# Kernel tuning notes

Hardware: AMD Instinct MI355X
Metric: run time of the kernel (lower is better)

Reference implementation:

```python
import jax, jax.numpy as jnp
import numpy as np

N, E, IN, H, G = 100000, 1600000, 64, 108, 128
N_LAYERS = 2  # hidden_dims=[108,108] -> 1 layer from hidden_dims[1:] + 1 final layer


def setup_inputs() -> dict:
    key = jax.random.key(0)
    ks = jax.random.split(key, 13)
    s = lambda fan_in: 1.0 / np.sqrt(fan_in)
    inp = {
        "nodes_feat": jax.random.normal(ks[0], (N, IN), jnp.float32),
        "edges_feat": jax.random.normal(ks[1], (E, 1), jnp.float32),
        "nodes_num_norm_sqrt": jax.random.uniform(ks[2], (N,), jnp.float32),
        "edges_num_norm_sqrt": jax.random.uniform(ks[3], (E,), jnp.float32),
        "W_emb": jax.random.uniform(ks[4], (IN, H), jnp.float32, -s(IN), s(IN)),
        "b_emb": jax.random.uniform(ks[5], (H,), jnp.float32, -s(IN), s(IN)),
        "pool_W": jax.random.uniform(ks[6], (N_LAYERS, H, H), jnp.float32, -s(H), s(H)),
        "pool_b": jax.random.uniform(ks[7], (N_LAYERS, H), jnp.float32, -s(H), s(H)),
        "app_W": jax.random.uniform(ks[8], (N_LAYERS, 2 * H, H), jnp.float32, -s(2 * H), s(2 * H)),
        "app_b": jax.random.uniform(ks[9], (N_LAYERS, H), jnp.float32, -s(2 * H), s(2 * H)),
        "src": jax.random.randint(ks[10], (E,), 0, N, jnp.int64 if jax.config.jax_enable_x64 else jnp.int32),
        "dst": jax.random.randint(ks[11], (E,), 0, N, jnp.int64 if jax.config.jax_enable_x64 else jnp.int32),
        "graph_ids": jnp.sort(jax.random.randint(ks[12], (N,), 0, G, jnp.int64 if jax.config.jax_enable_x64 else jnp.int32)),
        "n_graphs": G,
    }
    return inp


def reference(nodes_feat, edges_feat, nodes_num_norm_sqrt, edges_num_norm_sqrt,
              W_emb, b_emb, pool_W, pool_b, app_W, app_b,
              src, dst, graph_ids, n_graphs):
    n = nodes_feat.shape[0]
    # embedding_h
    h = nodes_feat @ W_emb + b_emb  # [N, H]
    # in-degree for mean aggregation (dropout = 0.0 so omitted)
    deg = jax.ops.segment_sum(jnp.ones((src.shape[0],), h.dtype), dst, num_segments=n)
    deg = jnp.maximum(deg, 1.0)[:, None]  # [N, 1]
    for i in range(pool_W.shape[0]):
        h_in = h
        # meanpool aggregator: per-message linear+ReLU == per-node transform then gather
        z = jax.nn.relu(h @ pool_W[i] + pool_b[i])  # [N, H]
        c = jax.ops.segment_sum(z[src], dst, num_segments=n) / deg  # mean over neighbors
        # NodeApply: linear(concat(h, c)) -> L2 normalize -> activation
        b = jnp.concatenate([h, c], axis=1) @ app_W[i] + app_b[i]
        b = b / jnp.maximum(jnp.linalg.norm(b, axis=1, keepdims=True), 1e-12)
        h = h_in + jax.nn.relu(b)  # residual (dims match: 108 == 108)
    # dgl.mean_nodes readout per graph
    cnt = jax.ops.segment_sum(jnp.ones((n,), h.dtype), graph_ids, num_segments=n_graphs)
    hg = jax.ops.segment_sum(h, graph_ids, num_segments=n_graphs) / jnp.maximum(cnt, 1.0)[:, None]
    return hg  # [n_graphs, H]
```

## Files before the change

kernel.cpp:

```cpp
#include <hip/hip_runtime.h>

#define HDIM 108
constexpr int G_GRAPHS = 128;
constexpr int MAXNB = 1024;
constexpr int CAP = 2560;

typedef _Float16 half8 __attribute__((ext_vector_type(8)));
typedef _Float16 half4v __attribute__((ext_vector_type(4)));
typedef float floatx4 __attribute__((ext_vector_type(4)));
typedef float floatx2 __attribute__((ext_vector_type(2)));

__device__ inline unsigned char f32_to_fp8(float t) {
#if __has_builtin(__builtin_amdgcn_cvt_pk_fp8_f32)
  return (unsigned char)(__builtin_amdgcn_cvt_pk_fp8_f32(t, t, 0, false) & 0xFF);
#else
  t = fminf(t, 448.f);
  if (t < 0.015625f) return (unsigned char)__float2int_rn(t * 512.f);
  unsigned u = __float_as_uint(t);
  unsigned lsb = (u >> 20) & 1;
  u += 0x7FFFFu + lsb;
  int e = (int)((u >> 23) & 0xFF) - 127;
  if (e > 8) return 0x7E;
  return (unsigned char)(((e + 7) << 3) | ((u >> 20) & 7));
#endif
}

template <bool HI>
__device__ inline floatx2 fp8x2_to_f32(unsigned v) {
#if __has_builtin(__builtin_amdgcn_cvt_pk_f32_fp8)
  return __builtin_amdgcn_cvt_pk_f32_fp8((int)v, HI);
#else
  unsigned b0 = HI ? ((v >> 16) & 0xFF) : (v & 0xFF);
  unsigned b1 = HI ? ((v >> 24) & 0xFF) : ((v >> 8) & 0xFF);
  floatx2 r;
  {
    unsigned s = b0 >> 7, e = (b0 >> 3) & 0xF, m = b0 & 7;
    float f = (e == 0) ? (float)m * 0.001953125f
                       : __uint_as_float(((e + 120u) << 23) | (m << 20));
    r[0] = s ? -f : f;
  }
  {
    unsigned s = b1 >> 7, e = (b1 >> 3) & 0xF, m = b1 & 7;
    float f = (e == 0) ? (float)m * 0.001953125f
                       : __uint_as_float(((e + 120u) << 23) | (m << 20));
    r[1] = s ? -f : f;
  }
  return r;
#endif
}

__global__ __launch_bounds__(1024) void k_scatter(const int* __restrict__ src, const int* __restrict__ dst,
                                                  int* __restrict__ gcur, int* __restrict__ ebuf,
                                                  const float* __restrict__ W_emb,
                                                  const float* __restrict__ pool_W,
                                                  const float* __restrict__ app_W,
                                                  _Float16* __restrict__ wte,
                                                  _Float16* __restrict__ wtp,
                                                  _Float16* __restrict__ wta,
                                                  int E, int nb) {
  __shared__ int hist[MAXNB];
  const int tid = threadIdx.x;
  const int e0 = blockIdx.x * 16384;

  int gi = blockIdx.x * 1024 + tid;
  if (gi < 86016) {
    const float* srcw;
    _Float16* dstw;
    int Kpad, K, split, rel;
    if (gi < 7168)       { rel = gi;          srcw = W_emb;          dstw = wte;         Kpad = 64;  K = 64;  split = 0; }
    else if (gi < 21504) { rel = gi - 7168;   srcw = pool_W;         dstw = wtp;         Kpad = 128; K = 108; split = 0; }
    else if (gi < 35840) { rel = gi - 21504;  srcw = pool_W + 11664; dstw = wtp + 14336; Kpad = 128; K = 108; split = 0; }
    else if (gi < 60928) { rel = gi - 35840;  srcw = app_W;          dstw = wta;         Kpad = 224; K = 216; split = 1; }
    else                 { rel = gi - 60928;  srcw = app_W + 23328;  dstw = wta + 25088; Kpad = 224; K = 216; split = 1; }
    int n = rel / Kpad, k = rel - n * Kpad;
    int ks;
    if (split) ks = (k < 108) ? k : (k >= 112 && k < 220) ? (k - 4) : -1;
    else       ks = (k < K) ? k : -1;
    float v = (n < 108 && ks >= 0) ? srcw[ks * 108 + n] : 0.f;
    dstw[rel] = (_Float16)v;
  }

  for (int b = tid; b < nb; b += 1024) hist[b] = 0;
  __syncthreads();
#pragma unroll
  for (int it = 0; it < 16; it++) {
    int e = e0 + it * 1024 + tid;
    if (e < E) atomicAdd(&hist[dst[e] >> 7], 1);
  }
  __syncthreads();
  for (int b = tid; b < nb; b += 1024) {
    int h = hist[b];
    hist[b] = h ? atomicAdd(&gcur[b * 16], h) : 0;
  }
  __syncthreads();
#pragma unroll
  for (int it = 0; it < 16; it++) {
    int e = e0 + it * 1024 + tid;
    if (e < E) {
      int d = dst[e];
      int b = d >> 7;
      int rank = atomicAdd(&hist[b], 1);
      if (rank < CAP) ebuf[(size_t)b * CAP + rank] = src[e] | ((d & 127) << 20);
    }
  }
}

__global__ __launch_bounds__(1024) void k_bagg(const unsigned char* __restrict__ z, const int* __restrict__ ebuf,
                                               const int* __restrict__ gcur, _Float16* __restrict__ c16,
                                               int N, int nb) {
  __shared__ int cnts[128];
  __shared__ int scanb[128];
  __shared__ int off[129];
  __shared__ int ecur[128];
  __shared__ int esrc[CAP];
  const int tid = threadIdx.x;
  const int b = blockIdx.x;
  const int v0 = b << 7;
  int cntb = gcur[b * 16];
  if (cntb > CAP) cntb = CAP;
  const int* eb = ebuf + (size_t)b * CAP;

  if (tid < 128) cnts[tid] = 0;
  __syncthreads();
  for (int i = tid; i < cntb; i += 1024) atomicAdd(&cnts[eb[i] >> 20], 1);
  __syncthreads();
  if (tid < 128) scanb[tid] = cnts[tid];
  __syncthreads();
#pragma unroll
  for (int st = 1; st < 128; st <<= 1) {
    int v = 0;
    if (tid < 128 && tid >= st) v = scanb[tid - st];
    __syncthreads();
    if (tid < 128) scanb[tid] += v;
    __syncthreads();
  }
  if (tid == 0) off[0] = 0;
  if (tid < 128) {
    off[tid + 1] = scanb[tid];
    ecur[tid] = scanb[tid] - cnts[tid];
  }
  __syncthreads();
  for (int i = tid; i < cntb; i += 1024) {
    int e = eb[i];
    int p = atomicAdd(&ecur[e >> 20], 1);
    esrc[p] = e & 0xFFFFF;
  }
  __syncthreads();

  const int lane = tid & 31;
  const int grp = tid >> 5;
  if (lane >= 28) return;
  const unsigned char* __restrict__ zl = z + lane * 4;
#pragma unroll 1
  for (int r = grp; r < 128; r += 32) {
    int v = v0 + r;
    if (v >= N) continue;
    int s = off[r], e2 = off[r + 1];
    float a0 = 0.f, a1 = 0.f, a2 = 0.f, a3 = 0.f;
    int j = s;
    for (; j + 4 <= e2; j += 4) {
      unsigned q0 = *(const unsigned*)(zl + (size_t)esrc[j] * 128);
      unsigned q1 = *(const unsigned*)(zl + (size_t)esrc[j + 1] * 128);
      unsigned q2 = *(const unsigned*)(zl + (size_t)esrc[j + 2] * 128);
      unsigned q3 = *(const unsigned*)(zl + (size_t)esrc[j + 3] * 128);
      floatx2 l0 = fp8x2_to_f32<false>(q0), h0 = fp8x2_to_f32<true>(q0);
      floatx2 l1 = fp8x2_to_f32<false>(q1), h1 = fp8x2_to_f32<true>(q1);
      floatx2 l2 = fp8x2_to_f32<false>(q2), h2 = fp8x2_to_f32<true>(q2);
      floatx2 l3 = fp8x2_to_f32<false>(q3), h3 = fp8x2_to_f32<true>(q3);
      a0 += (l0[0] + l1[0]) + (l2[0] + l3[0]);
      a1 += (l0[1] + l1[1]) + (l2[1] + l3[1]);
      a2 += (h0[0] + h1[0]) + (h2[0] + h3[0]);
      a3 += (h0[1] + h1[1]) + (h2[1] + h3[1]);
    }
    for (; j < e2; j++) {
      unsigned q0 = *(const unsigned*)(zl + (size_t)esrc[j] * 128);
      floatx2 l0 = fp8x2_to_f32<false>(q0), h0 = fp8x2_to_f32<true>(q0);
      a0 += l0[0]; a1 += l0[1]; a2 += h0[0]; a3 += h0[1];
    }
    int d = e2 - s;
    float inv = 1.f / (float)(d > 0 ? d : 1);
    half4v r4;
    r4[0] = (_Float16)(a0 * inv); r4[1] = (_Float16)(a1 * inv);
    r4[2] = (_Float16)(a2 * inv); r4[3] = (_Float16)(a3 * inv);
    *(half4v*)(c16 + (size_t)v * 112 + lane * 4) = r4;
  }
}

template <int KCH, int MODE>
__global__ __launch_bounds__(256) void k_mmf(const void* Asrc, const _Float16* __restrict__ c16,
                                             const _Float16* __restrict__ Wt, const float* __restrict__ bias,
                                             void* outp, int N) {
  constexpr int KW = KCH * 32;
  __shared__ _Float16 As[64 * 40];
  __shared__ _Float16 Ws[112 * 40];

  const int tid = threadIdx.x;
  const int wave = tid >> 6;
  const int lane = tid & 63;
  const int lo = lane & 15;
  const int quad = lane >> 4;
  const int n0 = blockIdx.x * 64;
  const _Float16* h16 = (const _Float16*)Asrc;
  const float* feat = (const float*)Asrc;

  floatx4 acc[7];
#pragma unroll
  for (int ct = 0; ct < 7; ct++) {
    floatx4 zz = {0.f, 0.f, 0.f, 0.f};
    acc[ct] = zz;
  }

#pragma unroll 1
  for (int kc = 0; kc < KCH; kc++) {
    {
      int r = tid >> 2, sg = tid & 3;
      int gn = n0 + r;
      int k = kc * 32 + sg * 8;
      half8 v = {0, 0, 0, 0, 0, 0, 0, 0};
      if (gn < N) {
        if (MODE == 0) {
          float4 f0 = *(const float4*)(feat + (size_t)gn * 64 + k);
          float4 f1 = *(const float4*)(feat + (size_t)gn * 64 + k + 4);
          v[0] = (_Float16)f0.x; v[1] = (_Float16)f0.y; v[2] = (_Float16)f0.z; v[3] = (_Float16)f0.w;
          v[4] = (_Float16)f1.x; v[5] = (_Float16)f1.y; v[6] = (_Float16)f1.z; v[7] = (_Float16)f1.w;
        } else if (MODE == 2) {
          const _Float16* sp = (k < 112) ? (h16 + (size_t)gn * 112 + k)
                                         : (c16 + (size_t)gn * 112 + (k - 112));
          v = *(const half8*)sp;
        } else {
          if (k < 112) v = *(const half8*)(h16 + (size_t)gn * 112 + k);
        }
      }
      *(half8*)&As[r * 40 + sg * 8] = v;
    }
#pragma unroll
    for (int it = 0; it < 2; it++) {
      int idx = tid + it * 256;
      if (idx < 448) {
        int nrow = idx >> 2, sg = idx & 3;
        half8 v = *(const half8*)(Wt + (size_t)nrow * KW + kc * 32 + sg * 8);
        *(half8*)&Ws[nrow * 40 + sg * 8] = v;
      }
    }
    __syncthreads();

    half8 a = *(const half8*)&As[(wave * 16 + lo) * 40 + quad * 8];
#pragma unroll
    for (int ct = 0; ct < 7; ct++) {
      half8 b = *(const half8*)&Ws[(ct * 16 + lo) * 40 + quad * 8];
      acc[ct] = __builtin_amdgcn_mfma_f32_16x16x32_f16(a, b, acc[ct], 0, 0, 0);
    }
    __syncthreads();
  }

  float bias_v[7];
#pragma unroll
  for (int ct = 0; ct < 7; ct++) {
    int col = ct * 16 + lo;
    bias_v[ct] = (col < 108) ? bias[col] : 0.f;
  }

  if (MODE == 2) {
    _Float16* out16 = (_Float16*)outp;
#pragma unroll
    for (int reg = 0; reg < 4; reg++) {
      int gr = n0 + wave * 16 + quad * 4 + reg;
      float bv[7];
      float ssq = 0.f;
#pragma unroll
      for (int ct = 0; ct < 7; ct++) {
        float t = acc[ct][reg] + bias_v[ct];
        bv[ct] = t;
        ssq += t * t;
      }
#pragma unroll
      for (int s = 1; s < 16; s <<= 1) ssq += __shfl_xor(ssq, s, 16);
      float scale = 1.f / fmaxf(sqrtf(ssq), 1e-12f);
      if (gr < N) {
        _Float16* hp = out16 + (size_t)gr * 112 + lo;
#pragma unroll
        for (int ct = 0; ct < 7; ct++) {
          float hv = (float)hp[ct * 16];
          hp[ct * 16] = (_Float16)(hv + fmaxf(bv[ct] * scale, 0.f));
        }
      }
    }
  } else if (MODE == 1) {
    unsigned char* outb = (unsigned char*)outp;
#pragma unroll
    for (int reg = 0; reg < 4; reg++) {
      int gr = n0 + wave * 16 + quad * 4 + reg;
      if (gr < N) {
        unsigned char* op = outb + (size_t)gr * 128 + lo;
#pragma unroll
        for (int ct = 0; ct < 7; ct++) {
          float t = fmaxf(acc[ct][reg] + bias_v[ct], 0.f);
          op[ct * 16] = f32_to_fp8(t);
        }
      }
    }
  } else {
    _Float16* out16 = (_Float16*)outp;
#pragma unroll
    for (int reg = 0; reg < 4; reg++) {
      int gr = n0 + wave * 16 + quad * 4 + reg;
      if (gr < N) {
        _Float16* op = out16 + (size_t)gr * 112 + lo;
#pragma unroll
        for (int ct = 0; ct < 7; ct++) {
          float t = acc[ct][reg] + bias_v[ct];
          op[ct * 16] = (_Float16)t;
        }
      }
    }
  }
}

__global__ __launch_bounds__(256) void k_readout(const _Float16* __restrict__ h, const int* __restrict__ gid,
                                                 float* __restrict__ hg, int N) {
  const int CH = 64;
  const int lane = threadIdx.x & 31;
  const int grp = threadIdx.x >> 5;
  int start = (blockIdx.x * 8 + grp) * CH;
  if (start >= N || lane >= 27) return;
  int end = min(start + CH, N);
  float a0 = 0.f, a1 = 0.f, a2 = 0.f, a3 = 0.f;
  int cur = gid[start];
  for (int i = start; i < end; i++) {
    int g = gid[i];
    if (g != cur) {
      float* base = &hg[(size_t)cur * HDIM + lane * 4];
      atomicAdd(base + 0, a0); atomicAdd(base + 1, a1);
      atomicAdd(base + 2, a2); atomicAdd(base + 3, a3);
      a0 = a1 = a2 = a3 = 0.f;
      cur = g;
    }
    half4v v = *(const half4v*)(h + (size_t)i * 112 + lane * 4);
    a0 += (float)v[0]; a1 += (float)v[1]; a2 += (float)v[2]; a3 += (float)v[3];
  }
  float* base = &hg[(size_t)cur * HDIM + lane * 4];
  atomicAdd(base + 0, a0); atomicAdd(base + 1, a1);
  atomicAdd(base + 2, a2); atomicAdd(base + 3, a3);
}

__global__ __launch_bounds__(256) void k_div(const float* __restrict__ hg, const int* __restrict__ gid,
                                             float* __restrict__ out, int total, int N) {
  int i = blockIdx.x * 256 + threadIdx.x;
  if (i < total) {
    int g = i / HDIM;
    int lo = 0, hi = N;
    while (lo < hi) { int m = (lo + hi) >> 1; if (gid[m] < g) lo = m + 1; else hi = m; }
    int lb = lo;
    lo = 0; hi = N;
    while (lo < hi) { int m = (lo + hi) >> 1; if (gid[m] <= g) lo = m + 1; else hi = m; }
    int c = lo - lb;
    out[i] = hg[i] / (float)(c > 0 ? c : 1);
  }
}

extern "C" void kernel_launch(void* const* d_in, const int* in_sizes, int n_in,
                              void* d_out, int out_size, void* d_ws, size_t ws_size,
                              hipStream_t stream) {
  (void)n_in; (void)ws_size; (void)out_size;
  const float* nodes_feat = (const float*)d_in[0];
  const float* W_emb = (const float*)d_in[4];
  const float* b_emb = (const float*)d_in[5];
  const float* pool_W = (const float*)d_in[6];
  const float* pool_b = (const float*)d_in[7];
  const float* app_W = (const float*)d_in[8];
  const float* app_b = (const float*)d_in[9];
  const int* src = (const int*)d_in[10];
  const int* dst = (const int*)d_in[11];
  const int* gid = (const int*)d_in[12];
  const int N = in_sizes[2];
  const int E = in_sizes[10];
  float* out = (float*)d_out;

  const int nb = (N + 127) >> 7;

  char* ws = (char*)d_ws;
  size_t off = 0;
  auto alloc = [&](size_t bytes) -> size_t {
    size_t o = off;
    off += (bytes + 1023) & ~size_t(1023);
    return o;
  };
  size_t o_gcur = alloc((size_t)MAXNB * 16 * 4);
  size_t o_hg   = alloc((size_t)G_GRAPHS * HDIM * 4);
  size_t zero_bytes = off;
  size_t o_ebuf = alloc((size_t)MAXNB * CAP * 4);
  size_t o_h  = alloc((size_t)N * 112 * 2);
  size_t o_z  = alloc((size_t)N * 128);
  size_t o_c  = alloc((size_t)N * 112 * 2);
  size_t o_we = alloc((size_t)112 * 64 * 2);
  size_t o_wp = alloc((size_t)2 * 112 * 128 * 2);
  size_t o_wa = alloc((size_t)2 * 112 * 224 * 2);

  int*           gcur = (int*)(ws + o_gcur);
  float*         hg   = (float*)(ws + o_hg);
  int*           ebuf = (int*)(ws + o_ebuf);
  _Float16*      h16  = (_Float16*)(ws + o_h);
  unsigned char* z8   = (unsigned char*)(ws + o_z);
  _Float16*      c16  = (_Float16*)(ws + o_c);
  _Float16*      wte  = (_Float16*)(ws + o_we);
  _Float16*      wtp  = (_Float16*)(ws + o_wp);
  _Float16*      wta  = (_Float16*)(ws + o_wa);

  (void)hipMemsetAsync(d_ws, 0, zero_bytes, stream);

  k_scatter<<<(E + 16383) / 16384, 1024, 0, stream>>>(src, dst, gcur, ebuf,
                                                      W_emb, pool_W, app_W,
                                                      wte, wtp, wta, E, nb);

  const int nbMM = (N + 63) / 64;
  k_mmf<2, 0><<<nbMM, 256, 0, stream>>>(nodes_feat, nullptr, wte, b_emb, h16, N);

  for (int i = 0; i < 2; i++) {
    k_mmf<4, 1><<<nbMM, 256, 0, stream>>>(h16, nullptr, wtp + i * 14336,
                                          pool_b + i * HDIM, z8, N);
    k_bagg<<<nb, 1024, 0, stream>>>(z8, ebuf, gcur, c16, N, nb);
    k_mmf<7, 2><<<nbMM, 256, 0, stream>>>(h16, c16, wta + i * 25088,
                                          app_b + i * HDIM, h16, N);
  }

  k_readout<<<(N + 8 * 64 - 1) / (8 * 64), 256, 0, stream>>>(h16, gid, hg, N);
  k_div<<<(G_GRAPHS * HDIM + 255) / 256, 256, 0, stream>>>(hg, gid, out, G_GRAPHS * HDIM, N);
}
```

Baseline: 337.3 us.

## Fuse edge scatter and embedding matmul into one heterogeneous kernel launch

Merges the edge-bucketing scatter kernel and the embedding GEMM into a single launch. The first blocks do the scatter and weight transposition, and the remaining blocks each run four 64-row embedding tiles, reading W_emb directly from fp32 instead of a pre-transposed copy. This removes one launch and lets the two independent phases overlap on the device. It also shrinks the readout chunk size so more threads share the final reduction, at the cost of more atomics.

```diff
diff --git a/kernel.cpp b/kernel.cpp
--- a/kernel.cpp
+++ b/kernel.cpp
@@ -49,58 +49,135 @@
 #endif
 }
 
-__global__ __launch_bounds__(1024) void k_scatter(const int* __restrict__ src, const int* __restrict__ dst,
-                                                  int* __restrict__ gcur, int* __restrict__ ebuf,
-                                                  const float* __restrict__ W_emb,
-                                                  const float* __restrict__ pool_W,
-                                                  const float* __restrict__ app_W,
-                                                  _Float16* __restrict__ wte,
-                                                  _Float16* __restrict__ wtp,
-                                                  _Float16* __restrict__ wta,
-                                                  int E, int nb) {
-  __shared__ int hist[MAXNB];
+__global__ __launch_bounds__(1024) void k_fused0(const int* __restrict__ src, const int* __restrict__ dst,
+                                                 int* __restrict__ gcur, int* __restrict__ ebuf,
+                                                 const float* __restrict__ pool_W,
+                                                 const float* __restrict__ app_W,
+                                                 _Float16* __restrict__ wtp,
+                                                 _Float16* __restrict__ wta,
+                                                 const float* __restrict__ feat,
+                                                 const float* __restrict__ W_emb,
+                                                 const float* __restrict__ b_emb,
+                                                 _Float16* __restrict__ h16,
+                                                 int E, int nb, int nsc, int N) {
+  __shared__ __align__(16) char smraw[29440];
   const int tid = threadIdx.x;
-  const int e0 = blockIdx.x * 16384;
-
-  int gi = blockIdx.x * 1024 + tid;
-  if (gi < 86016) {
-    const float* srcw;
-    _Float16* dstw;
-    int Kpad, K, split, rel;
-    if (gi < 7168)       { rel = gi;          srcw = W_emb;          dstw = wte;         Kpad = 64;  K = 64;  split = 0; }
-    else if (gi < 21504) { rel = gi - 7168;   srcw = pool_W;         dstw = wtp;         Kpad = 128; K = 108; split = 0; }
-    else if (gi < 35840) { rel = gi - 21504;  srcw = pool_W + 11664; dstw = wtp + 14336; Kpad = 128; K = 108; split = 0; }
-    else if (gi < 60928) { rel = gi - 35840;  srcw = app_W;          dstw = wta;         Kpad = 224; K = 216; split = 1; }
-    else                 { rel = gi - 60928;  srcw = app_W + 23328;  dstw = wta + 25088; Kpad = 224; K = 216; split = 1; }
-    int n = rel / Kpad, k = rel - n * Kpad;
-    int ks;
-    if (split) ks = (k < 108) ? k : (k >= 112 && k < 220) ? (k - 4) : -1;
-    else       ks = (k < K) ? k : -1;
-    float v = (n < 108 && ks >= 0) ? srcw[ks * 108 + n] : 0.f;
-    dstw[rel] = (_Float16)v;
-  }
-
-  for (int b = tid; b < nb; b += 1024) hist[b] = 0;
-  __syncthreads();
-#pragma unroll
-  for (int it = 0; it < 16; it++) {
-    int e = e0 + it * 1024 + tid;
-    if (e < E) atomicAdd(&hist[dst[e] >> 7], 1);
-  }
-  __syncthreads();
-  for (int b = tid; b < nb; b += 1024) {
-    int h = hist[b];
-    hist[b] = h ? atomicAdd(&gcur[b * 16], h) : 0;
-  }
-  __syncthreads();
-#pragma unroll
-  for (int it = 0; it < 16; it++) {
-    int e = e0 + it * 1024 + tid;
-    if (e < E) {
-      int d = dst[e];
-      int b = d >> 7;
-      int rank = atomicAdd(&hist[b], 1);
-      if (rank < CAP) ebuf[(size_t)b * CAP + rank] = src[e] | ((d & 127) << 20);
+
+  if ((int)blockIdx.x < nsc) {
+    int* hist = (int*)smraw;
+    const int e0 = blockIdx.x * 16384;
+
+    int gi = blockIdx.x * 1024 + tid;
+    if (gi < 78848) {
+      const float* srcw;
+      _Float16* dstw;
+      int Kpad, split, rel;
+      if (gi < 14336)      { rel = gi;          srcw = pool_W;         dstw = wtp;         Kpad = 128; split = 0; }
+      else if (gi < 28672) { rel = gi - 14336;  srcw = pool_W + 11664; dstw = wtp + 14336; Kpad = 128; split = 0; }
+      else if (gi < 53760) { rel = gi - 28672;  srcw = app_W;          dstw = wta;         Kpad = 224; split = 1; }
+      else                 { rel = gi - 53760;  srcw = app_W + 23328;  dstw = wta + 25088; Kpad = 224; split = 1; }
+      int n = rel / Kpad, k = rel - n * Kpad;
+      int ks;
+      if (split) ks = (k < 108) ? k : (k >= 112 && k < 220) ? (k - 4) : -1;
+      else       ks = (k < 108) ? k : -1;
+      float v = (n < 108 && ks >= 0) ? srcw[ks * 108 + n] : 0.f;
+      dstw[rel] = (_Float16)v;
+    }
+
+    for (int b = tid; b < nb; b += 1024) hist[b] = 0;
+    __syncthreads();
+#pragma unroll
+    for (int it = 0; it < 16; it++) {
+      int e = e0 + it * 1024 + tid;
+      if (e < E) atomicAdd(&hist[dst[e] >> 7], 1);
+    }
+    __syncthreads();
+    for (int b = tid; b < nb; b += 1024) {
+      int h = hist[b];
+      hist[b] = h ? atomicAdd(&gcur[b * 16], h) : 0;
+    }
+    __syncthreads();
+#pragma unroll
+    for (int it = 0; it < 16; it++) {
+      int e = e0 + it * 1024 + tid;
+      if (e < E) {
+        int d = dst[e];
+        int b = d >> 7;
+        int rank = atomicAdd(&hist[b], 1);
+        if (rank < CAP) ebuf[(size_t)b * CAP + rank] = src[e] | ((d & 127) << 20);
+      }
+    }
+  } else {
+    _Float16* As = (_Float16*)smraw;
+    _Float16* Ws = (_Float16*)(smraw + 20480);
+    const int sub = tid >> 8;
+    const int stid = tid & 255;
+    const int swave = stid >> 6;
+    const int slane = stid & 63;
+    const int lo = slane & 15;
+    const int quad = slane >> 4;
+    const int n0 = (((int)blockIdx.x - nsc) * 4 + sub) * 64;
+
+    floatx4 acc[7];
+#pragma unroll
+    for (int ct = 0; ct < 7; ct++) {
+      floatx4 zz = {0.f, 0.f, 0.f, 0.f};
+      acc[ct] = zz;
+    }
+
+#pragma unroll 1
+    for (int kc = 0; kc < 2; kc++) {
+      {
+        int r = stid >> 2, sg = stid & 3;
+        int gn = n0 + r;
+        int k = kc * 32 + sg * 8;
+        half8 v = {0, 0, 0, 0, 0, 0, 0, 0};
+        if (gn < N) {
+          float4 f0 = *(const float4*)(feat + (size_t)gn * 64 + k);
+          float4 f1 = *(const float4*)(feat + (size_t)gn * 64 + k + 4);
+          v[0] = (_Float16)f0.x; v[1] = (_Float16)f0.y; v[2] = (_Float16)f0.z; v[3] = (_Float16)f0.w;
+          v[4] = (_Float16)f1.x; v[5] = (_Float16)f1.y; v[6] = (_Float16)f1.z; v[7] = (_Float16)f1.w;
+        }
+        *(half8*)&As[sub * 2560 + r * 40 + sg * 8] = v;
+      }
+      if (tid < 448) {
+        int nrow = tid >> 2, sg = tid & 3;
+        int kb = kc * 32 + sg * 8;
+        half8 v = {0, 0, 0, 0, 0, 0, 0, 0};
+        if (nrow < 108) {
+#pragma unroll
+          for (int j = 0; j < 8; j++) v[j] = (_Float16)W_emb[(kb + j) * 108 + nrow];
+        }
+        *(half8*)&Ws[nrow * 40 + sg * 8] = v;
+      }
+      __syncthreads();
+
+      half8 a = *(const half8*)&As[sub * 2560 + (swave * 16 + lo) * 40 + quad * 8];
+#pragma unroll
+      for (int ct = 0; ct < 7; ct++) {
+        half8 b = *(const half8*)&Ws[(ct * 16 + lo) * 40 + quad * 8];
+        acc[ct] = __builtin_amdgcn_mfma_f32_16x16x32_f16(a, b, acc[ct], 0, 0, 0);
+      }
+      __syncthreads();
+    }
+
+    float bias_v[7];
+#pragma unroll
+    for (int ct = 0; ct < 7; ct++) {
+      int col = ct * 16 + lo;
+      bias_v[ct] = (col < 108) ? b_emb[col] : 0.f;
+    }
+#pragma unroll
+    for (int reg = 0; reg < 4; reg++) {
+      int gr = n0 + swave * 16 + quad * 4 + reg;
+      if (gr < N) {
+        _Float16* op = h16 + (size_t)gr * 112 + lo;
+#pragma unroll
+        for (int ct = 0; ct < 7; ct++) {
+          float t = acc[ct][reg] + bias_v[ct];
+          op[ct * 16] = (_Float16)t;
+        }
+      }
     }
   }
 }
@@ -201,7 +278,6 @@
   const int quad = lane >> 4;
   const int n0 = blockIdx.x * 64;
   const _Float16* h16 = (const _Float16*)Asrc;
-  const float* feat = (const float*)Asrc;
 
   floatx4 acc[7];
 #pragma unroll
@@ -218,12 +294,7 @@
       int k = kc * 32 + sg * 8;
       half8 v = {0, 0, 0, 0, 0, 0, 0, 0};
       if (gn < N) {
-        if (MODE == 0) {
-          float4 f0 = *(const float4*)(feat + (size_t)gn * 64 + k);
-          float4 f1 = *(const float4*)(feat + (size_t)gn * 64 + k + 4);
-          v[0] = (_Float16)f0.x; v[1] = (_Float16)f0.y; v[2] = (_Float16)f0.z; v[3] = (_Float16)f0.w;
-          v[4] = (_Float16)f1.x; v[5] = (_Float16)f1.y; v[6] = (_Float16)f1.z; v[7] = (_Float16)f1.w;
-        } else if (MODE == 2) {
+        if (MODE == 2) {
           const _Float16* sp = (k < 112) ? (h16 + (size_t)gn * 112 + k)
                                          : (c16 + (size_t)gn * 112 + (k - 112));
           v = *(const half8*)sp;
@@ -285,7 +356,7 @@
         }
       }
     }
-  } else if (MODE == 1) {
+  } else {
     unsigned char* outb = (unsigned char*)outp;
 #pragma unroll
     for (int reg = 0; reg < 4; reg++) {
@@ -299,26 +370,12 @@
         }
       }
     }
-  } else {
-    _Float16* out16 = (_Float16*)outp;
-#pragma unroll
-    for (int reg = 0; reg < 4; reg++) {
-      int gr = n0 + wave * 16 + quad * 4 + reg;
-      if (gr < N) {
-        _Float16* op = out16 + (size_t)gr * 112 + lo;
-#pragma unroll
-        for (int ct = 0; ct < 7; ct++) {
-          float t = acc[ct][reg] + bias_v[ct];
-          op[ct * 16] = (_Float16)t;
-        }
-      }
-    }
   }
 }
 
 __global__ __launch_bounds__(256) void k_readout(const _Float16* __restrict__ h, const int* __restrict__ gid,
                                                  float* __restrict__ hg, int N) {
-  const int CH = 64;
+  const int CH = 16;
   const int lane = threadIdx.x & 31;
   const int grp = threadIdx.x >> 5;
   int start = (blockIdx.x * 8 + grp) * CH;
@@ -377,6 +434,9 @@
   float* out = (float*)d_out;
 
   const int nb = (N + 127) >> 7;
+  const int nbMM = (N + 63) / 64;
+  const int nsc = (E + 16383) / 16384;
+  const int ngb = (nbMM + 3) / 4;
 
   char* ws = (char*)d_ws;
   size_t off = 0;
@@ -392,7 +452,6 @@
   size_t o_h  = alloc((size_t)N * 112 * 2);
   size_t o_z  = alloc((size_t)N * 128);
   size_t o_c  = alloc((size_t)N * 112 * 2);
-  size_t o_we = alloc((size_t)112 * 64 * 2);
   size_t o_wp = alloc((size_t)2 * 112 * 128 * 2);
   size_t o_wa = alloc((size_t)2 * 112 * 224 * 2);
 
@@ -402,18 +461,15 @@
   _Float16*      h16  = (_Float16*)(ws + o_h);
   unsigned char* z8   = (unsigned char*)(ws + o_z);
   _Float16*      c16  = (_Float16*)(ws + o_c);
-  _Float16*      wte  = (_Float16*)(ws + o_we);
   _Float16*      wtp  = (_Float16*)(ws + o_wp);
   _Float16*      wta  = (_Float16*)(ws + o_wa);
 
   (void)hipMemsetAsync(d_ws, 0, zero_bytes, stream);
 
-  k_scatter<<<(E + 16383) / 16384, 1024, 0, stream>>>(src, dst, gcur, ebuf,
-                                                      W_emb, pool_W, app_W,
-                                                      wte, wtp, wta, E, nb);
-
-  const int nbMM = (N + 63) / 64;
-  k_mmf<2, 0><<<nbMM, 256, 0, stream>>>(nodes_feat, nullptr, wte, b_emb, h16, N);
+  k_fused0<<<nsc + ngb, 1024, 0, stream>>>(src, dst, gcur, ebuf,
+                                           pool_W, app_W, wtp, wta,
+                                           nodes_feat, W_emb, b_emb, h16,
+                                           E, nb, nsc, N);
 
   for (int i = 0; i < 2; i++) {
     k_mmf<4, 1><<<nbMM, 256, 0, stream>>>(h16, nullptr, wtp + i * 14336,
@@ -423,6 +479,6 @@
                                           app_b + i * HDIM, h16, N);
   }
 
-  k_readout<<<(N + 8 * 64 - 1) / (8 * 64), 256, 0, stream>>>(h16, gid, hg, N);
+  k_readout<<<(N + 8 * 16 - 1) / (8 * 16), 256, 0, stream>>>(h16, gid, hg, N);
   k_div<<<(G_GRAPHS * HDIM + 255) / 256, 256, 0, stream>>>(hg, gid, out, G_GRAPHS * HDIM, N);
 }
```

New measurement: 328.6 us. 1.03x faster.
